# Kernel optimization log

Measured on AMD Instinct MI355X. Metric: run time of the kernel, lower is better.

Reference implementation:

```python
import jax, jax.numpy as jnp
import numpy as np

N_LAYER, MEM_LEN, D, V, B = 16, 512, 1024, 32000, 1
N_EVENTS, TOPK = 256, 40
NEG_INF = jnp.float32(-1e30)


def _model_step(tok, mems, E, Wl, Wo):
    # surrogate TransformerXL single-token step
    # tok: [B] int, mems: [L, MEM_LEN, B, D]
    h = E[tok]                                   # [B, D]
    ctx = mems[:, -1]                            # [L, B, D]
    h_new = jnp.tanh(jnp.einsum('bd,lde->lbe', h, Wl) + ctx)  # [L, B, D]
    logits = h_new[-1] @ Wo                      # [B, V]
    mems = jnp.concatenate([mems[:, 1:], h_new[:, None]], axis=1)
    return mems, logits


def setup_inputs() -> dict:
    key = jax.random.key(0)
    k1, k2, k3, k4 = jax.random.split(key, 4)
    return {
        'input_ids': jax.random.randint(k1, (128, B), 0, V),          # [T, B] seq-first prompt
        'E': jax.random.normal(k2, (V, D), jnp.float32) * 0.02,
        'Wl': jax.random.normal(k3, (N_LAYER, D, D), jnp.float32) * 0.02,
        'Wo': jax.random.normal(k4, (D, V), jnp.float32) * 0.02,
        'mems_init': jnp.zeros((N_LAYER, MEM_LEN, B, D), jnp.float32),
        'token_counts': jnp.zeros((B, V), jnp.int32),
        'temperature': jnp.float32(0.9),
        'repetition_penalty': jnp.float32(1.2),
        'n_events': N_EVENTS,
        'topk': TOPK,
    }


def reference(input_ids, E, Wl, Wo, mems_init, token_counts, temperature,
              repetition_penalty, n_events, topk):
    # ---- prompt processing fills the memories ----
    def pstep(mems, tok):
        mems, logits = _model_step(tok, mems, E, Wl, Wo)
        return mems, logits
    mems, prompt_logits = jax.lax.scan(pstep, mems_init, input_ids)
    pred_logits = prompt_logits[-1]                    # [B, V]

    keys = jax.random.split(jax.random.key(42), n_events)

    def gstep(carry, key_t):
        mems, counts, logits = carry
        l = logits / temperature
        # repetition penalty: divide logits of already-emitted tokens
        l = jnp.where(counts > 0, l / repetition_penalty, l)
        # top-k filter: keep logits >= k-th largest
        kth = jax.lax.top_k(l, topk)[0][:, -1:]        # [B, 1]
        lf = jnp.where(l < kth, NEG_INF, l)
        # multinomial(softmax(lf)) == categorical(lf)
        tok = jax.random.categorical(key_t, lf, axis=-1)  # [B]
        counts = counts.at[jnp.arange(B), tok].add(1)
        mems, logits = _model_step(tok, mems, E, Wl, Wo)
        return (mems, counts, logits), tok

    _, toks = jax.lax.scan(gstep, (mems, token_counts, pred_logits), keys)
    return toks.T.astype(jnp.int64)                    # [B, n_events]
```

## Files before the change

kernel.cpp:

```cpp
#include <hip/hip_runtime.h>
#include <hip/hip_cooperative_groups.h>
#include <cmath>

namespace cg = cooperative_groups;

#define JAX_PARTITIONABLE 1

#define NBLK 250
#define NTHR 1024
#define DIM 1024
#define VOCAB 32000
#define TPROMPT 128
#define NEVENTS 256
#define TOPK 40
#define CAP 2048


__device__ __forceinline__ void tf2x32(unsigned k0, unsigned k1, unsigned x0, unsigned x1,
                                       unsigned& o0, unsigned& o1) {
  unsigned ks2 = k0 ^ k1 ^ 0x1BD11BDAu;
  x0 += k0; x1 += k1;
#define TFR(r) { x0 += x1; x1 = (x1 << (r)) | (x1 >> (32 - (r))); x1 ^= x0; }
  TFR(13) TFR(15) TFR(26) TFR(6)
  x0 += k1; x1 += ks2 + 1u;
  TFR(17) TFR(29) TFR(16) TFR(24)
  x0 += ks2; x1 += k0 + 2u;
  TFR(13) TFR(15) TFR(26) TFR(6)
  x0 += k0; x1 += k1 + 3u;
  TFR(17) TFR(29) TFR(16) TFR(24)
  x0 += k1; x1 += ks2 + 4u;
  TFR(13) TFR(15) TFR(26) TFR(6)
  x0 += ks2; x1 += k0 + 5u;
#undef TFR
  o0 = x0; o1 = x1;
}

__device__ __forceinline__ float gumbel_f(unsigned k0, unsigned k1, unsigned v) {
#pragma clang fp contract(off)
  unsigned bits;
#if JAX_PARTITIONABLE
  unsigned y0, y1; tf2x32(k0, k1, 0u, v, y0, y1);
  bits = y0 ^ y1;
#else
  unsigned y0, y1;
  if (v < 16000u) { tf2x32(k0, k1, v, v + 16000u, y0, y1); bits = y0; }
  else            { tf2x32(k0, k1, v - 16000u, v, y0, y1); bits = y1; }
#endif
  const float TINYF = 1.1754943508222875e-38f;
  float f  = __uint_as_float((bits >> 9) | 0x3f800000u);
  float fl = f - 1.0f;
  float u  = fmaxf(TINYF, fl + TINYF);
  float t1 = (float)log((double)u);
  float t3 = (float)log((double)(-t1));
  return -t3;
}

__device__ __forceinline__ float xla_tanhf(float x) {
#pragma clang fp contract(off)
  const float kMax = 7.90531110763549805f;
  float xc = fminf(fmaxf(x, -kMax), kMax);
  float x2 = xc * xc;
  float num = xc * (4.89352455891786e-03f + x2 * (6.37261928875436e-04f +
              x2 * (1.48572235717979e-05f + x2 * (5.12229709037114e-08f +
              x2 * (-8.60467152213735e-11f + x2 * (2.00018790482477e-13f +
              x2 * (-2.76076847742355e-16f)))))));
  float den = 4.89352518554385e-03f + x2 * (2.26843463243900e-03f +
              x2 * (1.18534705686654e-04f + x2 * (1.19825839466702e-06f)));
  float r = num / den;
  return (fabsf(x) < 0.0004f) ? x : r;
}

__device__ __forceinline__ unsigned f2s(float x) {
  unsigned u = __float_as_uint(x);
  return (u & 0x80000000u) ? ~u : (u | 0x80000000u);
}
__device__ __forceinline__ float s2f(unsigned s) {
  unsigned u = (s & 0x80000000u) ? (s & 0x7fffffffu) : ~s;
  return __uint_as_float(u);
}

__device__ __forceinline__ void pick_bin_wave(const unsigned* s_h, int nb, int rank,
                                              int* dst, int tid) {
  if (tid < 64) {
    const int l = tid;
    const int per = (nb + 63) >> 6;
    const int base = l * per;
    unsigned lsum = 0;
    for (int b = 0; b < per; ++b) {
      int idx = base + b;
      if (idx < nb) lsum += s_h[idx];
    }
    unsigned suf = lsum;
#pragma unroll
    for (int off = 1; off < 64; off <<= 1) {
      unsigned o = __shfl_down(suf, off);
      if (l + off < 64) suf += o;
    }
    unsigned above = suf - lsum;
    if ((int)above < rank && (int)suf >= rank) {
      unsigned cum = above;
      for (int b = per - 1; b >= 0; --b) {
        int idx = base + b;
        if (idx >= nb) continue;
        unsigned c = s_h[idx];
        if ((int)cum < rank && (int)(cum + c) >= rank) {
          dst[0] = idx;
          dst[1] = rank - (int)cum;
        }
        cum += c;
      }
    }
  }
}

__device__ void logits_slice(int blk, int tid, int s, const float* Wo, const float* ctx,
                             const float* temp_p, const float* pen_p, const int* counts,
                             const unsigned* k256, unsigned* skey, float* marr,
                             unsigned* ghist, float* hs, double* s_pd, unsigned* s_h) {
  hs[tid] = ctx[tid];
  s_h[tid] = 0u; s_h[tid + 1024] = 0u;
  __syncthreads();
  const int vq = tid & 31, dg = tid >> 5;
  const int d0 = dg * 32;
  const float4* w4 = (const float4*)Wo + (size_t)d0 * (VOCAB / 4) + (blk * 32 + vq);
  double a0 = 0.0, a1 = 0.0, a2 = 0.0, a3 = 0.0;
#pragma unroll 16
  for (int j = 0; j < 32; ++j) {
    float4 w = w4[(size_t)j * (VOCAB / 4)];
    double h = (double)hs[d0 + j];
    a0 = fma(h, (double)w.x, a0);
    a1 = fma(h, (double)w.y, a1);
    a2 = fma(h, (double)w.z, a2);
    a3 = fma(h, (double)w.w, a3);
  }
  s_pd[dg * 128 + vq * 4 + 0] = a0;
  s_pd[dg * 128 + vq * 4 + 1] = a1;
  s_pd[dg * 128 + vq * 4 + 2] = a2;
  s_pd[dg * 128 + vq * 4 + 3] = a3;
  __syncthreads();
  if (tid < 128) {
#pragma clang fp contract(off)
    double acc = 0.0;
#pragma unroll
    for (int dgi = 0; dgi < 32; ++dgi) acc += s_pd[dgi * 128 + tid];
    int v = blk * 128 + tid;
    float lg = (float)acc;
    float l1 = lg / (*temp_p);
    if (counts[v] > 0) l1 = l1 / (*pen_p);
    unsigned key = f2s(l1);
    skey[v] = key;
    float g = gumbel_f(k256[2 * s], k256[2 * s + 1], (unsigned)v);
    marr[v] = l1 + g;
    atomicAdd(&s_h[key >> 21], 1u);
  }
  __syncthreads();
  {
    unsigned c;
    c = s_h[tid];        if (c) atomicAdd(&ghist[tid], c);
    c = s_h[tid + 1024]; if (c) atomicAdd(&ghist[tid + 1024], c);
  }
  __syncthreads();
}

__device__ void layer_slice(int lblk, int tid, int i, const float* E, const float* Wl15,
                            float* ctx, int* misc, float* hs, double* s_rd, int* s_misc) {
  if (tid == 0) {
    int spins = 0;
    while (__hip_atomic_load(misc + 16, __ATOMIC_RELAXED, __HIP_MEMORY_SCOPE_AGENT) < i + 1) {
      __builtin_amdgcn_s_sleep(2);
      if (++spins > (1 << 20)) break;
    }
    while (__hip_atomic_load(misc + 16, __ATOMIC_ACQUIRE, __HIP_MEMORY_SCOPE_AGENT) < i + 1)
      __builtin_amdgcn_s_sleep(8);
    s_misc[7] = misc[0];
  }
  __syncthreads();
  const int tok = s_misc[7];
  const float* erow = E + (size_t)tok * DIM;
  hs[tid] = erow[tid];
  __syncthreads();
  const int eL = tid & 63, dg = tid >> 6;
  const int e = (lblk << 6) + eL;
  const float* w = Wl15 + (size_t)(dg * 64) * DIM + e;
  double acc = 0.0;
#pragma unroll 16
  for (int j = 0; j < 64; ++j)
    acc = fma((double)hs[dg * 64 + j], (double)w[(size_t)j * DIM], acc);
  s_rd[dg * 64 + eL] = acc;
  __syncthreads();
  if (tid < 64) {
    double a = 0.0;
#pragma unroll
    for (int dgi = 0; dgi < 16; ++dgi) a += s_rd[dgi * 64 + tid];
    float sv = (float)a + ctx[(lblk << 6) + tid];
    ctx[(lblk << 6) + tid] = xla_tanhf(sv);
  }
  __syncthreads();
}

__device__ void sampler_phase(int i, const unsigned* skey, const float* marr,
                              int* counts, int* out, unsigned* ghist, int* misc,
                              unsigned* s_h, float* s_val, int* s_idx,
                              unsigned* s_ck, int* s_cv, float* s_cm, int* s_misc) {
  const int tid = threadIdx.x;
  if (tid == 0) s_misc[3] = 0;
  if (tid < 512) {
    const uint4* gh4 = (const uint4*)ghist;
    uint4 h4 = gh4[tid];
    s_h[4 * tid + 0] = h4.x; s_h[4 * tid + 1] = h4.y;
    s_h[4 * tid + 2] = h4.z; s_h[4 * tid + 3] = h4.w;
  }
  __syncthreads();

  pick_bin_wave(s_h, 2048, TOPK, &s_misc[0], tid);
  __syncthreads();
  const int B = s_misc[0];
  int rr = s_misc[1];

  float bm = -INFINITY; int bv = 0x7fffffff;
  const uint4* sk4 = (const uint4*)skey;
  const float4* mr4 = (const float4*)marr;
  for (int g = tid; g < VOCAB / 4; g += NTHR) {
    uint4 k4 = sk4[g];
    float4 m4 = mr4[g];
    unsigned kk[4] = { k4.x, k4.y, k4.z, k4.w };
    float mm[4] = { m4.x, m4.y, m4.z, m4.w };
#pragma unroll
    for (int c = 0; c < 4; ++c) {
      int b = (int)(kk[c] >> 21);
      int v = 4 * g + c;
      if (b > B) {
        if (mm[c] > bm || (mm[c] == bm && v < bv)) { bm = mm[c]; bv = v; }
      } else if (b == B) {
        int pos = atomicAdd(&s_misc[3], 1);
        if (pos < CAP) { s_ck[pos] = kk[c]; s_cv[pos] = v; s_cm[pos] = mm[c]; }
      }
    }
  }
  __syncthreads();
  const int cc = s_misc[3];
  unsigned pref = ((unsigned)B) << 21;
  const int sh_arr[3] = { 13, 5, 0 };
  const unsigned him_arr[3] = { 0xFFE00000u, 0xFFFFE000u, 0xFFFFFFE0u };
  const int nb_arr[3] = { 256, 256, 32 };
  const bool fits = (cc <= CAP);
  for (int p = 0; p < 3; ++p) {
    const int sh = sh_arr[p];
    const unsigned him = him_arr[p];
    const int nb = nb_arr[p];
    if (tid < nb) s_h[tid] = 0u;
    __syncthreads();
    if (fits) {
      for (int j = tid; j < cc; j += NTHR) {
        unsigned k = s_ck[j];
        if ((k & him) == pref) atomicAdd(&s_h[(k >> sh) & (unsigned)(nb - 1)], 1u);
      }
    } else {
      for (int v = tid; v < VOCAB; v += NTHR) {
        unsigned k = skey[v];
        if ((k & him) == pref) atomicAdd(&s_h[(k >> sh) & (unsigned)(nb - 1)], 1u);
      }
    }
    __syncthreads();
    pick_bin_wave(s_h, nb, rr, &s_misc[4], tid);
    __syncthreads();
    pref |= ((unsigned)s_misc[4]) << sh;
    rr = s_misc[5];
    __syncthreads();
  }
  const unsigned kth = pref;

  if (fits) {
    for (int j = tid; j < cc; j += NTHR) {
      if (s_ck[j] >= kth) {
        float m = s_cm[j]; int v = s_cv[j];
        if (m > bm || (m == bm && v < bv)) { bm = m; bv = v; }
      }
    }
  } else {
    for (int v = tid; v < VOCAB; v += NTHR) {
      if (skey[v] >= kth) {
        float m = marr[v];
        if (m > bm || (m == bm && v < bv)) { bm = m; bv = v; }
      }
    }
  }
  for (int g = tid; g < 2048; g += NTHR) ghist[g] = 0u;

  s_val[tid] = bm; s_idx[tid] = bv;
  __syncthreads();
  for (int s = NTHR / 2; s > 0; s >>= 1) {
    if (tid < s) {
      float ov = s_val[tid + s]; int oi = s_idx[tid + s];
      if (ov > s_val[tid] || (ov == s_val[tid] && oi < s_idx[tid])) {
        s_val[tid] = ov; s_idx[tid] = oi;
      }
    }
    __syncthreads();
  }
  if (tid == 0) {
    int tok = s_idx[0];
    counts[tok] += 1;
    out[i] = tok;
    misc[0] = tok;
    __hip_atomic_fetch_add(misc + 16, 1, __ATOMIC_RELEASE, __HIP_MEMORY_SCOPE_AGENT);
  }
  __syncthreads();
}

__global__ void __launch_bounds__(NTHR, 1) tfxl_kernel(
    const int* __restrict__ ids, const float* __restrict__ E,
    const float* __restrict__ Wl, const float* __restrict__ Wo,
    const float* __restrict__ mems, const int* __restrict__ tcin,
    const float* __restrict__ temp_p, const float* __restrict__ pen_p,
    int* __restrict__ out,
    float* __restrict__ Ht, float* __restrict__ ctx,
    unsigned* __restrict__ skey, float* __restrict__ marr,
    int* __restrict__ counts, unsigned* __restrict__ k256,
    int* __restrict__ misc, unsigned* __restrict__ ghist) {
  cg::grid_group grid = cg::this_grid();
  const int tid = threadIdx.x;
  const int blk = blockIdx.x;

  __shared__ double smA[5120];
  __shared__ float hs[DIM];
  __shared__ double s_rd[NTHR];
  __shared__ unsigned s_h[2048];
  __shared__ float s_val[NTHR];
  __shared__ int s_idx[NTHR];
  __shared__ int s_misc[8];

  double* s_pd = smA;
  unsigned* s_ck = (unsigned*)smA;
  int* s_cv = (int*)(s_ck + CAP);
  float* s_cm = (float*)(s_cv + CAP);
  const float* Wl15 = Wl + (size_t)15 * DIM * DIM;

  {
    const int gsz = NBLK * NTHR;
    for (int g = blk * NTHR + tid; g < DIM * TPROMPT; g += gsz) {
      int t = g & 127, d = g >> 7;
      Ht[g] = E[(size_t)ids[t] * DIM + d];
    }
    int g = blk * NTHR + tid;
    if (g < DIM) ctx[g] = mems[((size_t)15 * 512 + 511) * DIM + g];
    if (g < VOCAB) counts[g] = tcin[g];
    if (g < NEVENTS) {
#if JAX_PARTITIONABLE
      unsigned y0, y1; tf2x32(0u, 42u, 0u, (unsigned)g, y0, y1);
      k256[2 * g] = y0; k256[2 * g + 1] = y1;
#else
      unsigned y0, y1, z0, z1;
      if (g < 128) {
        tf2x32(0u, 42u, (unsigned)(2 * g),     (unsigned)(2 * g + 256), y0, y1);
        tf2x32(0u, 42u, (unsigned)(2 * g + 1), (unsigned)(2 * g + 257), z0, z1);
        k256[2 * g] = y0; k256[2 * g + 1] = z0;
      } else {
        tf2x32(0u, 42u, (unsigned)(2 * g - 256), (unsigned)(2 * g),     y0, y1);
        tf2x32(0u, 42u, (unsigned)(2 * g - 255), (unsigned)(2 * g + 1), z0, z1);
        k256[2 * g] = y1; k256[2 * g + 1] = z1;
      }
#endif
    }
    if (g < 2048) ghist[g] = 0u;
    if (g < 256) misc[g] = 0;
  }
  grid.sync();

  if (blk < 16) {
    float* sc = (float*)smA;
    int eL = tid & 63, tg = tid >> 6;
    int e = (blk << 6) + eL;
    const float* wl = Wl15 + e;
    const float* hbase = Ht + tg * 8;
    double acc[8];
#pragma unroll
    for (int k = 0; k < 8; ++k) acc[k] = 0.0;
    for (int d = 0; d < DIM; ++d) {
      float w = wl[(size_t)d * DIM];
      const float* hrow = hbase + d * 128;
#pragma unroll
      for (int k = 0; k < 8; ++k)
        acc[k] = fma((double)hrow[k], (double)w, acc[k]);
    }
#pragma unroll
    for (int k = 0; k < 8; ++k)
      sc[eL * 129 + tg * 8 + k] = (float)acc[k];
    __syncthreads();
    if (tid < 64) {
      float sv = ctx[(blk << 6) + tid];
      for (int t = 0; t < TPROMPT; ++t)
        sv = xla_tanhf(sc[tid * 129 + t] + sv);
      ctx[(blk << 6) + tid] = sv;
    }
    __syncthreads();
  }
  grid.sync();

  logits_slice(blk, tid, 0, Wo, ctx, temp_p, pen_p, counts, k256,
               skey, marr, ghist, hs, s_pd, s_h);
  grid.sync();

  for (int i = 0; i < NEVENTS; ++i) {
    if (blk == 0)
      sampler_phase(i, skey, marr, counts, out, ghist, misc,
                    s_h, s_val, s_idx, s_ck, s_cv, s_cm, s_misc);
    if (i == NEVENTS - 1) break;
    if (blk >= 1 && blk <= 16)
      layer_slice(blk - 1, tid, i, E, Wl15, ctx, misc, hs, s_rd, s_misc);
    grid.sync();
    logits_slice(blk, tid, i + 1, Wo, ctx, temp_p, pen_p, counts, k256,
                 skey, marr, ghist, hs, s_pd, s_h);
    grid.sync();
  }
}

extern "C" void kernel_launch(void* const* d_in, const int* in_sizes, int n_in,
                              void* d_out, int out_size, void* d_ws, size_t ws_size,
                              hipStream_t stream) {
  const int*   ids  = (const int*)d_in[0];
  const float* E    = (const float*)d_in[1];
  const float* Wl   = (const float*)d_in[2];
  const float* Wo   = (const float*)d_in[3];
  const float* mems = (const float*)d_in[4];
  const int*   tcin = (const int*)d_in[5];
  const float* temp = (const float*)d_in[6];
  const float* pen  = (const float*)d_in[7];
  int* out = (int*)d_out;

  char* ws = (char*)d_ws;
  float*    Ht     = (float*)(ws + 0);
  float*    ctx    = (float*)(ws + 524288);
  unsigned* skey   = (unsigned*)(ws + 589824);
  float*    marr   = (float*)(ws + 720896);
  int*      counts = (int*)(ws + 851968);
  unsigned* k256   = (unsigned*)(ws + 979968);
  int*      misc   = (int*)(ws + 982016);
  unsigned* ghist  = (unsigned*)(ws + 983040);

  void* args[] = { &ids, &E, &Wl, &Wo, &mems, &tcin, &temp, &pen, &out,
                   &Ht, &ctx, &skey, &marr, &counts, &k256, &misc, &ghist };
  hipLaunchCooperativeKernel((const void*)tfxl_kernel, dim3(NBLK), dim3(NTHR),
                             (void**)args, 0, stream);
}
```

Before: 25.41 ms.

## Replace mid-step grid sync with layer counters and add speculative candidate list

The grid.sync after the layer update is replaced by per-block release counters on four striped words, which every block polls before computing its logits slice. Logits blocks also append any vocab entry whose key clears a speculative threshold, taken from the previous step's rank-160 bin, to a compact global list via wave ballot and atomics. The sampler then scans that short list instead of all 32000 entries whenever the list fits and the threshold is at or below the top-k bin. This removes one grid-wide barrier per step and cuts the sampler's memory sweep, at the cost of extra global atomics, spinning on global counters, and reusing the Ht buffer for the list.

```diff
diff --git a/kernel.cpp b/kernel.cpp
--- a/kernel.cpp
+++ b/kernel.cpp
@@ -14,6 +14,8 @@
 #define NEVENTS 256
 #define TOPK 40
 #define CAP 2048
+#define CAP_LIST 4096
+#define RSPEC 160
 
 
 __device__ __forceinline__ void tf2x32(unsigned k0, unsigned k1, unsigned x0, unsigned x1,
@@ -116,7 +118,9 @@
 __device__ void logits_slice(int blk, int tid, int s, const float* Wo, const float* ctx,
                              const float* temp_p, const float* pen_p, const int* counts,
                              const unsigned* k256, unsigned* skey, float* marr,
-                             unsigned* ghist, float* hs, double* s_pd, unsigned* s_h) {
+                             unsigned* ghist, int* misc,
+                             unsigned* gck, int* gcv, float* gcm,
+                             float* hs, double* s_pd, unsigned* s_h) {
   hs[tid] = ctx[tid];
   s_h[tid] = 0u; s_h[tid + 1024] = 0u;
   __syncthreads();
@@ -150,8 +154,23 @@
     unsigned key = f2s(l1);
     skey[v] = key;
     float g = gumbel_f(k256[2 * s], k256[2 * s + 1], (unsigned)v);
-    marr[v] = l1 + g;
+    float m = l1 + g;
+    marr[v] = m;
     atomicAdd(&s_h[key >> 21], 1u);
+    unsigned tspec = (unsigned)misc[112];
+    bool p = (key >= tspec);
+    unsigned long long bal = __ballot(p);
+    int lane = tid & 63;
+    int base = 0;
+    if (lane == 0) {
+      int cnt = (int)__popcll(bal);
+      if (cnt) base = atomicAdd(misc + 96, cnt);
+    }
+    base = __shfl(base, 0);
+    if (p) {
+      int pos = base + (int)__popcll(bal & ((1ULL << lane) - 1ULL));
+      if (pos < CAP_LIST) { gck[pos] = key; gcv[pos] = v; gcm[pos] = m; }
+    }
   }
   __syncthreads();
   {
@@ -168,7 +187,7 @@
     int spins = 0;
     while (__hip_atomic_load(misc + 16, __ATOMIC_RELAXED, __HIP_MEMORY_SCOPE_AGENT) < i + 1) {
       __builtin_amdgcn_s_sleep(2);
-      if (++spins > (1 << 20)) break;
+      if (++spins > (1 << 22)) break;
     }
     while (__hip_atomic_load(misc + 16, __ATOMIC_ACQUIRE, __HIP_MEMORY_SCOPE_AGENT) < i + 1)
       __builtin_amdgcn_s_sleep(8);
@@ -196,10 +215,14 @@
     ctx[(lblk << 6) + tid] = xla_tanhf(sv);
   }
   __syncthreads();
+  if (tid == 0)
+    __hip_atomic_fetch_add(misc + 32 + 16 * (lblk & 3), 1,
+                           __ATOMIC_RELEASE, __HIP_MEMORY_SCOPE_AGENT);
 }
 
 __device__ void sampler_phase(int i, const unsigned* skey, const float* marr,
                               int* counts, int* out, unsigned* ghist, int* misc,
+                              const unsigned* gck, const int* gcv, const float* gcm,
                               unsigned* s_h, float* s_val, int* s_idx,
                               unsigned* s_ck, int* s_cv, float* s_cm, int* s_misc) {
   const int tid = threadIdx.x;
@@ -213,27 +236,46 @@
   __syncthreads();
 
   pick_bin_wave(s_h, 2048, TOPK, &s_misc[0], tid);
+  pick_bin_wave(s_h, 2048, RSPEC, &s_misc[5], tid);
   __syncthreads();
   const int B = s_misc[0];
   int rr = s_misc[1];
+  const int bt = s_misc[5];
+  const int nc = misc[96];
+  const unsigned tspec = (unsigned)misc[112];
+  const bool fast = (nc <= CAP_LIST) && (tspec <= ((unsigned)B << 21));
 
   float bm = -INFINITY; int bv = 0x7fffffff;
-  const uint4* sk4 = (const uint4*)skey;
-  const float4* mr4 = (const float4*)marr;
-  for (int g = tid; g < VOCAB / 4; g += NTHR) {
-    uint4 k4 = sk4[g];
-    float4 m4 = mr4[g];
-    unsigned kk[4] = { k4.x, k4.y, k4.z, k4.w };
-    float mm[4] = { m4.x, m4.y, m4.z, m4.w };
-#pragma unroll
-    for (int c = 0; c < 4; ++c) {
-      int b = (int)(kk[c] >> 21);
-      int v = 4 * g + c;
+  if (fast) {
+    for (int j = tid; j < nc; j += NTHR) {
+      unsigned k = gck[j];
+      int b = (int)(k >> 21);
       if (b > B) {
-        if (mm[c] > bm || (mm[c] == bm && v < bv)) { bm = mm[c]; bv = v; }
+        float m = gcm[j]; int v = gcv[j];
+        if (m > bm || (m == bm && v < bv)) { bm = m; bv = v; }
       } else if (b == B) {
         int pos = atomicAdd(&s_misc[3], 1);
-        if (pos < CAP) { s_ck[pos] = kk[c]; s_cv[pos] = v; s_cm[pos] = mm[c]; }
+        if (pos < CAP) { s_ck[pos] = k; s_cv[pos] = gcv[j]; s_cm[pos] = gcm[j]; }
+      }
+    }
+  } else {
+    const uint4* sk4 = (const uint4*)skey;
+    const float4* mr4 = (const float4*)marr;
+    for (int g = tid; g < VOCAB / 4; g += NTHR) {
+      uint4 k4 = sk4[g];
+      float4 m4 = mr4[g];
+      unsigned kk[4] = { k4.x, k4.y, k4.z, k4.w };
+      float mm[4] = { m4.x, m4.y, m4.z, m4.w };
+#pragma unroll
+      for (int c = 0; c < 4; ++c) {
+        int b = (int)(kk[c] >> 21);
+        int v = 4 * g + c;
+        if (b > B) {
+          if (mm[c] > bm || (mm[c] == bm && v < bv)) { bm = mm[c]; bv = v; }
+        } else if (b == B) {
+          int pos = atomicAdd(&s_misc[3], 1);
+          if (pos < CAP) { s_ck[pos] = kk[c]; s_cv[pos] = v; s_cm[pos] = mm[c]; }
+        }
       }
     }
   }
@@ -284,6 +326,10 @@
         if (m > bm || (m == bm && v < bv)) { bm = m; bv = v; }
       }
     }
+  }
+  if (tid == 0) {
+    misc[112] = (int)(((unsigned)bt) << 21);
+    misc[96] = 0;
   }
   for (int g = tid; g < 2048; g += NTHR) ghist[g] = 0u;
 
@@ -335,6 +381,9 @@
   int* s_cv = (int*)(s_ck + CAP);
   float* s_cm = (float*)(s_cv + CAP);
   const float* Wl15 = Wl + (size_t)15 * DIM * DIM;
+  unsigned* gck = (unsigned*)Ht;
+  int*      gcv = (int*)(Ht + CAP_LIST);
+  float*    gcm = (float*)(Ht + 2 * CAP_LIST);
 
   {
     const int gsz = NBLK * NTHR;
@@ -363,7 +412,8 @@
 #endif
     }
     if (g < 2048) ghist[g] = 0u;
-    if (g < 256) misc[g] = 0;
+    if (g == 112) misc[g] = (int)0xFFFFFFFFu;
+    else if (g < 256) misc[g] = 0;
   }
   grid.sync();
 
@@ -398,19 +448,42 @@
   grid.sync();
 
   logits_slice(blk, tid, 0, Wo, ctx, temp_p, pen_p, counts, k256,
-               skey, marr, ghist, hs, s_pd, s_h);
+               skey, marr, ghist, misc, gck, gcv, gcm, hs, s_pd, s_h);
   grid.sync();
 
   for (int i = 0; i < NEVENTS; ++i) {
     if (blk == 0)
-      sampler_phase(i, skey, marr, counts, out, ghist, misc,
+      sampler_phase(i, skey, marr, counts, out, ghist, misc, gck, gcv, gcm,
                     s_h, s_val, s_idx, s_ck, s_cv, s_cm, s_misc);
     if (i == NEVENTS - 1) break;
     if (blk >= 1 && blk <= 16)
       layer_slice(blk - 1, tid, i, E, Wl15, ctx, misc, hs, s_rd, s_misc);
-    grid.sync();
+    if (tid == 0) {
+      const int target = 16 * (i + 1);
+      int spins = 0;
+      for (;;) {
+        int sacc = 0;
+#pragma unroll
+        for (int j = 0; j < 4; ++j)
+          sacc += __hip_atomic_load(misc + 32 + 16 * j, __ATOMIC_RELAXED,
+                                    __HIP_MEMORY_SCOPE_AGENT);
+        if (sacc >= target) break;
+        __builtin_amdgcn_s_sleep(8);
+        if (++spins > (1 << 22)) break;
+      }
+      for (;;) {
+        int sacc = 0;
+#pragma unroll
+        for (int j = 0; j < 4; ++j)
+          sacc += __hip_atomic_load(misc + 32 + 16 * j, __ATOMIC_ACQUIRE,
+                                    __HIP_MEMORY_SCOPE_AGENT);
+        if (sacc >= target) break;
+        __builtin_amdgcn_s_sleep(16);
+      }
+    }
+    __syncthreads();
     logits_slice(blk, tid, i + 1, Wo, ctx, temp_p, pen_p, counts, k256,
-                 skey, marr, ghist, hs, s_pd, s_h);
+                 skey, marr, ghist, misc, gck, gcv, gcm, hs, s_pd, s_h);
     grid.sync();
   }
 }
```

Measured after the change: 23.46 ms. -7.7%, faster.
